# Performance work log

Measured on AMD Instinct MI355X. Metric: run time of the kernel, lower is better.

## Reference

```python
import jax, jax.numpy as jnp
import numpy as np
from jax import lax

G, CPG, KS, N = 8, 8, 3, 9  # groups, channels per group, kernel size, ks*ks


def conv2d(x, w, b=None, pad=1):
    y = lax.conv_general_dilated(x, w, (1, 1), [(pad, pad), (pad, pad)],
                                 dimension_numbers=('NCHW', 'OIHW', 'NCHW'))
    if b is not None:
        y = y + b[None, :, None, None]
    return y


def deform_group(x, f, pw, pb, mw, mb, cw):
    # x: sampled feature (anchor slice), f: offset source (motion slice); both (b,c,h,w)
    b, c, h, w = x.shape
    offset = conv2d(f, pw, pb)                      # (b, 2N, h, w)
    m = jax.nn.sigmoid(conv2d(f, mw, mb))           # (b, N, h, w) modulation
    off = jnp.transpose(offset, (0, 2, 3, 1))       # (b, h, w, 2N): first N rows(x), last N cols(y)
    rng = jnp.arange(-1, 2, dtype=x.dtype)
    pn_x = jnp.repeat(rng, KS)                      # kernel row offset, n = kr*3 + kc
    pn_y = jnp.tile(rng, KS)                        # kernel col offset
    p0_x = jnp.arange(1, h + 1, dtype=x.dtype)[:, None, None]  # base grid starts at 1 (padding=0 here)
    p0_y = jnp.arange(1, w + 1, dtype=x.dtype)[None, :, None]
    px = p0_x + pn_x + off[..., :N]                 # (b, h, w, N)
    py = p0_y + pn_y + off[..., N:]
    fx = jnp.floor(lax.stop_gradient(px))           # p.detach().floor() in the original
    fy = jnp.floor(lax.stop_gradient(py))
    qx_lt = jnp.clip(fx, 0, h - 1)
    qx_rb = jnp.clip(fx + 1, 0, h - 1)
    qy_lt = jnp.clip(fy, 0, w - 1)
    qy_rb = jnp.clip(fy + 1, 0, w - 1)
    px = jnp.clip(px, 0, h - 1)
    py = jnp.clip(py, 0, w - 1)
    g_lt = (1 + (qx_lt - px)) * (1 + (qy_lt - py))
    g_rb = (1 - (qx_rb - px)) * (1 - (qy_rb - py))
    g_lb = (1 + (qx_lt - px)) * (1 - (qy_rb - py))
    g_rt = (1 - (qx_rb - px)) * (1 + (qy_lt - py))
    x_flat = x.reshape(b, c, h * w)

    def gather(ix, iy):
        idx = (ix * w + iy).astype(jnp.int32).reshape(b, 1, -1)  # (b,1,h*w*N)
        return jnp.take_along_axis(x_flat, idx, axis=2).reshape(b, c, h, w, N)

    x_off = (g_lt[:, None] * gather(qx_lt, qy_lt) + g_rb[:, None] * gather(qx_rb, qy_rb)
             + g_lb[:, None] * gather(qx_lt, qy_rb) + g_rt[:, None] * gather(qx_rb, qy_lt))
    x_off = x_off * jnp.transpose(m, (0, 2, 3, 1))[:, None]      # apply modulation mask
    # fused equivalent of reshape to (b,c,h*3,w*3) + conv(k=3, stride=3, no bias)
    return jnp.einsum('bchwn,ocn->bohw', x_off, cw.reshape(cw.shape[0], c, N))


def reference(o, anchor, pw, pb, mw, mb, cw, w1, b1, w2, b2):
    b, C, h, w = anchor.shape
    xg = anchor.reshape(b, G, CPG, h, w).transpose(1, 0, 2, 3, 4)  # (G,b,c,h,w)
    fg = o.reshape(b, G, CPG, h, w).transpose(1, 0, 2, 3, 4)
    tg = jax.vmap(deform_group)(xg, fg, pw, pb, mw, mb, cw)        # (G,b,c,h,w)
    target = tg.transpose(1, 0, 2, 3, 4).reshape(b, C, h, w)
    target_ = jnp.concatenate([target, anchor], axis=1)            # (b,128,h,w)
    return target + conv2d(conv2d(target_, w1, b1), w2, b2)


def setup_inputs() -> dict:
    key = jax.random.key(0)
    ks = jax.random.split(key, 11)
    B, C, H, W = 4, 64, 128, 128
    return {
        'o': jax.random.normal(ks[0], (B, C, H, W), jnp.float32),
        'anchor': jax.random.normal(ks[1], (B, C, H, W), jnp.float32),
        'pw': jax.random.normal(ks[2], (G, 2 * N, CPG, 3, 3), jnp.float32) * 0.05,
        'pb': jax.random.normal(ks[3], (G, 2 * N), jnp.float32) * 0.05,
        'mw': jax.random.normal(ks[4], (G, N, CPG, 3, 3), jnp.float32) * 0.05,
        'mb': jax.random.normal(ks[5], (G, N), jnp.float32) * 0.05,
        'cw': jax.random.normal(ks[6], (G, CPG, CPG, 3, 3), jnp.float32) * 0.05,
        'w1': jax.random.normal(ks[7], (64, 128, 3, 3), jnp.float32) * 0.05,
        'b1': jax.random.normal(ks[8], (64,), jnp.float32) * 0.05,
        'w2': jax.random.normal(ks[9], (64, 64, 3, 3), jnp.float32) * 0.05,
        'b2': jax.random.normal(ks[10], (64,), jnp.float32) * 0.05,
    }
```

## Files before the change

kernel.cpp:

```cpp
#include <hip/hip_runtime.h>


typedef __attribute__((ext_vector_type(8))) short short8;
typedef __attribute__((ext_vector_type(4))) float float4v;
typedef __attribute__((ext_vector_type(2))) float float2v;

#define MFMA_B16(a, b, c) __builtin_amdgcn_mfma_f32_16x16x32_bf16(a, b, c, 0, 0, 0)

__device__ __forceinline__ ushort f2bf(float f) {
    union { float f; unsigned u; } v; v.f = f;
    unsigned r = v.u + 0x7FFFu + ((v.u >> 16) & 1u);
    return (ushort)(r >> 16);
}
__device__ __forceinline__ float bf2f(ushort h) {
    union { unsigned u; float f; } v; v.u = ((unsigned)h) << 16;
    return v.f;
}

__device__ __forceinline__ void tap_wo(int gy, int gx, int n,
                                       float ox, float oy, float mzv,
                                       float* W, int* O)
{
    int ky = n / 3, kx = n - ky * 3;
    float pxf = (float)(gy + ky) + ox;
    float pyf = (float)(gx + kx) + oy;
    float fx = floorf(pxf), fy = floorf(pyf);
    float qxl = fminf(fmaxf(fx, 0.f), 127.f);
    float qxr = fminf(fmaxf(fx + 1.f, 0.f), 127.f);
    float qyl = fminf(fmaxf(fy, 0.f), 127.f);
    float qyr = fminf(fmaxf(fy + 1.f, 0.f), 127.f);
    float pxc = fminf(fmaxf(pxf, 0.f), 127.f);
    float pyc = fminf(fmaxf(pyf, 0.f), 127.f);
    float glx = 1.f + (qxl - pxc), grx = 1.f - (qxr - pxc);
    float gly = 1.f + (qyl - pyc), gry = 1.f - (qyr - pyc);
    float mm = 1.f / (1.f + __expf(-mzv));
    W[0] = glx * gly * mm; W[1] = grx * gry * mm;
    W[2] = glx * gry * mm; W[3] = grx * gly * mm;
    int ixl = (int)qxl, ixr = (int)qxr, iyl = (int)qyl, iyr = (int)qyr;
    O[0] = ixl * 128 + iyl; O[1] = ixr * 128 + iyr;
    O[2] = ixl * 128 + iyr; O[3] = ixr * 128 + iyl;
}

__device__ __forceinline__ short8 interp4(const float* W, const short8* cv)
{
    union U { short8 s; uint4 u; };
    uint4 c[4];
    #pragma unroll
    for (int j = 0; j < 4; ++j) { U t; t.s = cv[j]; c[j] = t.u; }
    U out;
    #pragma unroll
    for (int p = 0; p < 4; ++p) {
        float2v acc = {0.f, 0.f};
        #pragma unroll
        for (int j = 0; j < 4; ++j) {
            unsigned d = (&c[j].x)[p];
            float2v cc = {__uint_as_float(d << 16),
                          __uint_as_float(d & 0xffff0000u)};
            float2v Wv = {W[j], W[j]};
            acc = __builtin_elementwise_fma(cc, Wv, acc);
        }
        unsigned u0 = __float_as_uint(acc.x), u1 = __float_as_uint(acc.y);
        (&out.u.x)[p] = __builtin_amdgcn_perm(u1, u0, 0x07060302u);
    }
    return out.s;
}

__global__ __launch_bounds__(256) void prep(
    const float* __restrict__ anchor,
    const float* __restrict__ w1, const float* __restrict__ w2,
    const float* __restrict__ pw, const float* __restrict__ pb,
    const float* __restrict__ mw, const float* __restrict__ mb,
    const float* __restrict__ cw,
    ushort* __restrict__ anc_g,
    ushort* __restrict__ rw1, ushort* __restrict__ rw2,
    ushort* __restrict__ rpwh, ushort* __restrict__ rpwl,
    ushort* __restrict__ rcw)
{
    const int blk = blockIdx.x;
    if (blk < 256) {
        int pix = (blk & 63) * 256 + threadIdx.x;
        int b = blk >> 6;
        ushort tmp[64];
        #pragma unroll
        for (int ch = 0; ch < 64; ++ch)
            tmp[ch] = f2bf(anchor[(((size_t)(b * 64 + ch)) << 14) + pix]);
        #pragma unroll
        for (int grp = 0; grp < 8; ++grp) {
            short8 v;
            #pragma unroll
            for (int j = 0; j < 8; ++j) v[j] = (short)tmp[grp * 8 + j];
            *(short8*)(anc_g + ((size_t)(b * 8 + grp)) * 131072 + (size_t)pix * 8) = v;
        }
        return;
    }
    int i = (blk - 256) * 256 + threadIdx.x;
    if (i < 73728) {
        int kk = i & 31, r = i >> 5, oc = r & 63, r2 = r >> 6;
        int ks = r2 & 3, s = r2 >> 2, ic = ks * 32 + kk;
        rw1[i] = f2bf(w1[(oc * 128 + ic) * 9 + s]);
    }
    if (i < 36864) {
        int kk = i & 31, r = i >> 5, oc = r & 63, r2 = r >> 6;
        int ks = r2 & 1, s = r2 >> 1, ic = ks * 32 + kk;
        rw2[i] = f2bf(w2[(oc * 64 + ic) * 9 + s]);
    }
    if (i < 24576) {
        int kk = i & 31, r = i >> 5, n = r & 31, r2 = r >> 5;
        int ks = r2 % 3, g = r2 / 3, k = ks * 32 + kk;
        float v = 0.f;
        if (k < 72) {
            int s = k >> 3, ic = k & 7;
            if (n < 18)      v = pw[((g * 18 + n) * 8 + ic) * 9 + s];
            else if (n < 27) v = mw[((g * 9 + (n - 18)) * 8 + ic) * 9 + s];
        } else if (k == 72) {
            if (n < 18)      v = pb[g * 18 + n];
            else if (n < 27) v = mb[g * 9 + (n - 18)];
        }
        ushort h = f2bf(v);
        rpwh[i] = h;
        rpwl[i] = f2bf(v - bf2f(h));
    }
    if (i < 12288) {
        int kk = i & 31, r = i >> 5, oc = r & 15, r2 = r >> 4;
        int ks = r2 % 3, g = r2 / 3, k = ks * 32 + kk;
        float v = 0.f;
        if (k < 72 && oc < 8) {
            int n = k >> 3, ic = k & 7;
            v = cw[((g * 8 + oc) * 8 + ic) * 9 + n];
        }
        rcw[i] = f2bf(v);
    }
}

__global__ __launch_bounds__(256, 4) void deform_mfma(
    const float* __restrict__ o, const ushort* __restrict__ anc_g,
    const ushort* __restrict__ rpwh, const ushort* __restrict__ rpwl,
    const ushort* __restrict__ rcw,
    ushort* __restrict__ xcat_g, float* __restrict__ target)
{
    const int tile = blockIdx.x, g = blockIdx.y, b = blockIdx.z;
    const int ty0 = (tile >> 3) * 16, tx0 = (tile & 7) * 16;
    const int tid = threadIdx.x, lane = tid & 63, wave = tid >> 6;
    const int l15 = lane & 15, quad = lane >> 4;

    __shared__ __align__(16) ushort sU[19008];
    ushort* slabh = sU;
    ushort* slabl = sU + 2592;
    float*  sOff  = (float*)((char*)sU + 10368);
    float*  sEp   = (float*)sU;

    for (int idx = tid; idx < 8 * 324; idx += 256) {
        int ic = idx / 324; int pix = idx - ic * 324;
        int r = pix / 18, c = pix - r * 18;
        int gy = ty0 + r - 1, gx = tx0 + c - 1;
        float v = 0.f;
        if ((unsigned)gy < 128u && (unsigned)gx < 128u)
            v = o[(((size_t)(b * 64 + g * 8 + ic)) << 14) + (gy << 7) + gx];
        ushort h = f2bf(v);
        slabh[pix * 8 + ic] = h;
        slabl[pix * 8 + ic] = f2bf(v - bf2f(h));
    }
    __syncthreads();

    float4v offacc[4][2] = {};
    #pragma unroll
    for (int ks = 0; ks < 3; ++ks) {
        short8 Bh[2], Bl[2];
        #pragma unroll
        for (int nf = 0; nf < 2; ++nf) {
            int off = ((g * 3 + ks) * 32 + nf * 16 + l15) * 32 + quad * 8;
            Bh[nf] = *(const short8*)(rpwh + off);
            Bl[nf] = *(const short8*)(rpwl + off);
        }
        short8 Ah[4], Al[4];
        if (ks < 2) {
            int s = ks * 4 + quad, sy = s / 3, sx = s - sy * 3;
            #pragma unroll
            for (int py = 0; py < 4; ++py) {
                int row = wave * 4 + py;
                int sl = ((row + sy) * 18 + l15 + sx) * 8;
                Ah[py] = *(const short8*)(&slabh[sl]);
                Al[py] = *(const short8*)(&slabl[sl]);
            }
        } else {
            #pragma unroll
            for (int py = 0; py < 4; ++py) {
                short8 zh = {0, 0, 0, 0, 0, 0, 0, 0};
                short8 zl = {0, 0, 0, 0, 0, 0, 0, 0};
                if (quad == 0) {
                    int row = wave * 4 + py;
                    int sl = ((row + 2) * 18 + l15 + 2) * 8;
                    zh = *(const short8*)(&slabh[sl]);
                    zl = *(const short8*)(&slabl[sl]);
                } else if (quad == 1) {
                    zh[0] = (short)0x3F80;
                }
                Ah[py] = zh; Al[py] = zl;
            }
        }
        #pragma unroll
        for (int py = 0; py < 4; ++py)
            #pragma unroll
            for (int nf = 0; nf < 2; ++nf) {
                offacc[py][nf] = MFMA_B16(Ah[py], Bh[nf], offacc[py][nf]);
                offacc[py][nf] = MFMA_B16(Ah[py], Bl[nf], offacc[py][nf]);
                offacc[py][nf] = MFMA_B16(Al[py], Bh[nf], offacc[py][nf]);
            }
    }
    #pragma unroll
    for (int py = 0; py < 4; ++py) {
        int p0 = (wave * 4 + py) * 16 + quad * 4;
        #pragma unroll
        for (int nf = 0; nf < 2; ++nf) {
            int ch = nf * 16 + l15;
            if (ch < 27) {
                #pragma unroll
                for (int reg = 0; reg < 4; ++reg)
                    sOff[(p0 + reg) * 27 + ch] = offacc[py][nf][reg];
            }
        }
    }

    short8 Bw[3];
    #pragma unroll
    for (int ks = 0; ks < 3; ++ks)
        Bw[ks] = *(const short8*)(rcw + (((g * 3 + ks) * 16 + l15) * 32 + quad * 8));

    const ushort* gb = anc_g + ((size_t)(b * 8 + g)) * 131072;
    const int n1 = quad, n2 = quad + 4;
    float4v cacc[4] = {};
    #pragma unroll
    for (int py = 0; py < 4; ++py) {
        int prow = wave * 4 + py;
        int p = prow * 16 + l15;
        int gy = ty0 + prow, gx = tx0 + l15;

        float W[8]; int O[8];
        tap_wo(gy, gx, n1, sOff[p * 27 + n1], sOff[p * 27 + 9 + n1],
               sOff[p * 27 + 18 + n1], &W[0], &O[0]);
        tap_wo(gy, gx, n2, sOff[p * 27 + n2], sOff[p * 27 + 9 + n2],
               sOff[p * 27 + 18 + n2], &W[4], &O[4]);
        short8 cv[8];
        #pragma unroll
        for (int j = 0; j < 8; ++j)
            cv[j] = *(const short8*)(gb + (size_t)O[j] * 8);
        short8 A0 = interp4(&W[0], &cv[0]);
        short8 A1 = interp4(&W[4], &cv[4]);
        short8 A2 = {0, 0, 0, 0, 0, 0, 0, 0};
        if (quad == 0) {
            float W2[4]; int O2[4];
            tap_wo(gy, gx, 8, sOff[p * 27 + 8], sOff[p * 27 + 17],
                   sOff[p * 27 + 26], W2, O2);
            short8 c2[4];
            #pragma unroll
            for (int j = 0; j < 4; ++j)
                c2[j] = *(const short8*)(gb + (size_t)O2[j] * 8);
            A2 = interp4(W2, c2);
        }
        cacc[py] = MFMA_B16(A0, Bw[0], cacc[py]);
        cacc[py] = MFMA_B16(A1, Bw[1], cacc[py]);
        cacc[py] = MFMA_B16(A2, Bw[2], cacc[py]);
    }

    __syncthreads();
    #pragma unroll
    for (int py = 0; py < 4; ++py) {
        if (l15 < 8) {
            #pragma unroll
            for (int reg = 0; reg < 4; ++reg)
                sEp[((wave * 4 + py) * 16 + quad * 4 + reg) * 8 + l15] = cacc[py][reg];
        }
    }
    __syncthreads();
    {
        const int p = tid;
        const int gy = ty0 + (p >> 4), gx = tx0 + (p & 15);
        float res[8];
        #pragma unroll
        for (int oc = 0; oc < 8; ++oc) res[oc] = sEp[p * 8 + oc];
        short8 pk;
        #pragma unroll
        for (int oc = 0; oc < 8; ++oc) pk[oc] = (short)f2bf(res[oc]);
        *(short8*)(xcat_g + ((size_t)(b * 8 + g)) * 131072
                   + (size_t)((gy << 7) + gx) * 8) = pk;
        #pragma unroll
        for (int oc = 0; oc < 8; ++oc)
            target[(((size_t)(b * 64 + g * 8 + oc)) << 14) + (gy << 7) + gx] = res[oc];
    }
}

__global__ __launch_bounds__(256, 4) void conv1_mfma(
    const ushort* __restrict__ xg, const ushort* __restrict__ ag,
    const ushort* __restrict__ rw1, const float* __restrict__ b1,
    ushort* __restrict__ t1)
{
    const int patch = blockIdx.x, b = blockIdx.y;
    const int px0 = (patch & 7) * 16, py0 = (patch >> 3) * 8;
    const int tid = threadIdx.x, lane = tid & 63, wave = tid >> 6;
    const int mhalf = wave & 1, nhalf = wave >> 1;
    const int l15 = lane & 15, quad = lane >> 4;

    __shared__ __align__(16) ushort sA[180 * 72];

    float4v acc[4][2] = {};
    #pragma unroll
    for (int ph = 0; ph < 2; ++ph) {
        if (ph) __syncthreads();
        const ushort* src = (ph == 0) ? xg : ag;
        for (int task = tid; task < 1440; task += 256) {
            int grp = task / 180, pix = task - grp * 180;
            int r = pix / 18, c = pix - r * 18;
            int gy = py0 + r - 1, gx = px0 + c - 1;
            short8 v = {0, 0, 0, 0, 0, 0, 0, 0};
            if ((unsigned)gy < 128u && (unsigned)gx < 128u) {
                const ushort* plane = src + ((size_t)(b * 8 + grp)) * 131072;
                v = *(const short8*)(plane + (size_t)((gy << 7) + gx) * 8);
            }
            *(short8*)(&sA[pix * 72 + grp * 8]) = v;
        }
        __syncthreads();

        #pragma unroll
        for (int ks2 = 0; ks2 < 2; ++ks2) {
            const int ks = ph * 2 + ks2;
            #pragma unroll
            for (int ky = 0; ky < 3; ++ky) {
                short8 Bf[3][2];
                #pragma unroll
                for (int kx = 0; kx < 3; ++kx)
                    #pragma unroll
                    for (int nf = 0; nf < 2; ++nf) {
                        int oc = nhalf * 32 + nf * 16 + l15;
                        Bf[kx][nf] = *(const short8*)(rw1 +
                            ((((ky * 3 + kx) * 4 + ks) * 64 + oc) * 32 + quad * 8));
                    }
                #pragma unroll
                for (int py = 0; py < 4; ++py) {
                    int slabrow = mhalf * 4 + py + ky;
                    #pragma unroll
                    for (int kx = 0; kx < 3; ++kx) {
                        short8 A = *(const short8*)(&sA[(slabrow * 18 + l15 + kx) * 72
                                                        + ks2 * 32 + quad * 8]);
                        #pragma unroll
                        for (int nf = 0; nf < 2; ++nf)
                            acc[py][nf] = MFMA_B16(A, Bf[kx][nf], acc[py][nf]);
                    }
                }
            }
        }
    }
    __syncthreads();
    ushort* sE = sA;
    #pragma unroll
    for (int nf = 0; nf < 2; ++nf) {
        int oc = nhalf * 32 + nf * 16 + l15;
        float bias = b1[oc];
        #pragma unroll
        for (int py = 0; py < 4; ++py) {
            int row = mhalf * 4 + py;
            #pragma unroll
            for (int reg = 0; reg < 4; ++reg)
                sE[(row * 16 + quad * 4 + reg) * 64 + oc] = f2bf(acc[py][nf][reg] + bias);
        }
    }
    __syncthreads();
    {
        const size_t nbase = ((size_t)b) << 20;
        int pix = tid >> 1, half = tid & 1;
        int gy = py0 + (pix >> 4), gx = px0 + (pix & 15);
        ushort* dst = t1 + nbase + (size_t)((gy << 7) + gx) * 64 + half * 32;
        const ushort* sp = sE + pix * 64 + half * 32;
        #pragma unroll
        for (int j = 0; j < 4; ++j)
            *(short8*)(dst + j * 8) = *(const short8*)(sp + j * 8);
    }
}

__global__ __launch_bounds__(256, 4) void conv2_mfma(
    const ushort* __restrict__ t1, const ushort* __restrict__ rw2,
    const float* __restrict__ b2, float* outres)
{
    const int patch = blockIdx.x, b = blockIdx.y;
    const int px0 = (patch & 7) * 16, py0 = (patch >> 3) * 8;
    const int tid = threadIdx.x, lane = tid & 63, wave = tid >> 6;
    const int ohalf = wave & 1, rhalf = wave >> 1;
    const int l15 = lane & 15, quad = lane >> 4;

    __shared__ __align__(16) ushort sX[180 * 72];

    const size_t nbase = ((size_t)b) << 20;
    for (int task = tid; task < 1440; task += 256) {
        int pix = task >> 3, grp = task & 7;
        int r = pix / 18, c = pix - r * 18;
        int gy = py0 + r - 1, gx = px0 + c - 1;
        short8 v = {0, 0, 0, 0, 0, 0, 0, 0};
        if ((unsigned)gy < 128u && (unsigned)gx < 128u)
            v = *(const short8*)(t1 + nbase + (size_t)((gy << 7) + gx) * 64 + grp * 8);
        *(short8*)(&sX[pix * 72 + grp * 8]) = v;
    }
    __syncthreads();

    float4v acc[2][4] = {};
    #pragma unroll
    for (int ks = 0; ks < 2; ++ks) {
        #pragma unroll
        for (int ky = 0; ky < 3; ++ky) {
            short8 Aw[3][2];
            #pragma unroll
            for (int kx = 0; kx < 3; ++kx)
                #pragma unroll
                for (int mf = 0; mf < 2; ++mf) {
                    int oc = ohalf * 32 + mf * 16 + l15;
                    Aw[kx][mf] = *(const short8*)(rw2 +
                        ((((ky * 3 + kx) * 2 + ks) * 64 + oc) * 32 + quad * 8));
                }
            #pragma unroll
            for (int py = 0; py < 4; ++py) {
                int slabrow = rhalf * 4 + py + ky;
                #pragma unroll
                for (int kx = 0; kx < 3; ++kx) {
                    short8 Bx = *(const short8*)(&sX[(slabrow * 18 + l15 + kx) * 72
                                                     + ks * 32 + quad * 8]);
                    #pragma unroll
                    for (int mf = 0; mf < 2; ++mf)
                        acc[mf][py] = MFMA_B16(Aw[kx][mf], Bx, acc[mf][py]);
                }
            }
        }
    }
    #pragma unroll
    for (int mf = 0; mf < 2; ++mf)
        #pragma unroll
        for (int reg = 0; reg < 4; ++reg) {
            int oc = ohalf * 32 + mf * 16 + quad * 4 + reg;
            float bias = b2[oc];
            #pragma unroll
            for (int py = 0; py < 4; ++py) {
                int gy = py0 + rhalf * 4 + py, gx = px0 + l15;
                size_t idx = (((size_t)(b * 64 + oc)) << 14) + (gy << 7) + gx;
                outres[idx] = acc[mf][py][reg] + bias + outres[idx];
            }
        }
}

extern "C" void kernel_launch(void* const* d_in, const int* in_sizes, int n_in,
                              void* d_out, int out_size, void* d_ws, size_t ws_size,
                              hipStream_t stream) {
    const float* o      = (const float*)d_in[0];
    const float* anchor = (const float*)d_in[1];
    const float* pw     = (const float*)d_in[2];
    const float* pb     = (const float*)d_in[3];
    const float* mw     = (const float*)d_in[4];
    const float* mb     = (const float*)d_in[5];
    const float* cw     = (const float*)d_in[6];
    const float* w1     = (const float*)d_in[7];
    const float* b1     = (const float*)d_in[8];
    const float* w2     = (const float*)d_in[9];
    const float* b2     = (const float*)d_in[10];
    float* out = (float*)d_out;

    char* ws = (char*)d_ws;
    ushort* anc_g  = (ushort*)(ws);
    ushort* xcat_g = (ushort*)(ws + 8388608);
    ushort* t1b    = (ushort*)(ws + 16777216);
    char*   wsm    = ws + 25165824;
    ushort* rw1p   = (ushort*)(wsm);
    ushort* rw2p   = (ushort*)(wsm + 147456);
    ushort* rpwh   = (ushort*)(wsm + 147456 + 73728);
    ushort* rpwl   = (ushort*)(wsm + 147456 + 73728 + 49152);
    ushort* rcwp   = (ushort*)(wsm + 147456 + 73728 + 98304);

    prep<<<544, 256, 0, stream>>>(anchor, w1, w2, pw, pb, mw, mb, cw,
                                  anc_g, rw1p, rw2p, rpwh, rpwl, rcwp);
    deform_mfma<<<dim3(64, 8, 4), 256, 0, stream>>>(o, anc_g, rpwh, rpwl, rcwp,
                                                    xcat_g, out );
    conv1_mfma<<<dim3(128, 4), 256, 0, stream>>>(xcat_g, anc_g, rw1p, b1, t1b);
    conv2_mfma<<<dim3(128, 4), 256, 0, stream>>>(t1b, rw2p, b2, out);
}
```

Baseline: 175.1 us.

## Drop fp32 target write; read bf16 residual from xcat in conv2

The deform kernel no longer writes the fp32 target tensor to the output buffer. conv2 instead reads the residual from the bf16 xcat buffer, removing one fp32 write and one fp32 read of the output. The deform slab load now has each thread load all 8 channels of a pixel and store them as packed short8 vectors. The residual added to the output is now bf16-rounded instead of fp32, which reduces accuracy.

```diff
diff --git a/kernel.cpp b/kernel.cpp
--- a/kernel.cpp
+++ b/kernel.cpp
@@ -136,7 +136,7 @@
     const float* __restrict__ o, const ushort* __restrict__ anc_g,
     const ushort* __restrict__ rpwh, const ushort* __restrict__ rpwl,
     const ushort* __restrict__ rcw,
-    ushort* __restrict__ xcat_g, float* __restrict__ target)
+    ushort* __restrict__ xcat_g)
 {
     const int tile = blockIdx.x, g = blockIdx.y, b = blockIdx.z;
     const int ty0 = (tile >> 3) * 16, tx0 = (tile & 7) * 16;
@@ -147,18 +147,30 @@
     ushort* slabh = sU;
     ushort* slabl = sU + 2592;
     float*  sOff  = (float*)((char*)sU + 10368);
-    float*  sEp   = (float*)sU;
-
-    for (int idx = tid; idx < 8 * 324; idx += 256) {
-        int ic = idx / 324; int pix = idx - ic * 324;
-        int r = pix / 18, c = pix - r * 18;
-        int gy = ty0 + r - 1, gx = tx0 + c - 1;
-        float v = 0.f;
-        if ((unsigned)gy < 128u && (unsigned)gx < 128u)
-            v = o[(((size_t)(b * 64 + g * 8 + ic)) << 14) + (gy << 7) + gx];
-        ushort h = f2bf(v);
-        slabh[pix * 8 + ic] = h;
-        slabl[pix * 8 + ic] = f2bf(v - bf2f(h));
+    ushort* sEu   = sU;
+
+    const float* obase = o + (((size_t)(b * 64 + g * 8)) << 14);
+    #pragma unroll
+    for (int pass = 0; pass < 2; ++pass) {
+        int pix = tid + pass * 256;
+        if (pix < 324) {
+            int r = pix / 18, c = pix - r * 18;
+            int gy = ty0 + r - 1, gx = tx0 + c - 1;
+            short8 vh = {0, 0, 0, 0, 0, 0, 0, 0};
+            short8 vl = {0, 0, 0, 0, 0, 0, 0, 0};
+            if ((unsigned)gy < 128u && (unsigned)gx < 128u) {
+                const float* p0 = obase + (gy << 7) + gx;
+                #pragma unroll
+                for (int ic = 0; ic < 8; ++ic) {
+                    float v = p0[(size_t)ic << 14];
+                    ushort h = f2bf(v);
+                    vh[ic] = (short)h;
+                    vl[ic] = (short)f2bf(v - bf2f(h));
+                }
+            }
+            *(short8*)(&slabh[pix * 8]) = vh;
+            *(short8*)(&slabl[pix * 8]) = vl;
+        }
     }
     __syncthreads();
 
@@ -268,24 +280,16 @@
         if (l15 < 8) {
             #pragma unroll
             for (int reg = 0; reg < 4; ++reg)
-                sEp[((wave * 4 + py) * 16 + quad * 4 + reg) * 8 + l15] = cacc[py][reg];
+                sEu[((wave * 4 + py) * 16 + quad * 4 + reg) * 8 + l15] =
+                    f2bf(cacc[py][reg]);
         }
     }
     __syncthreads();
     {
-        const int p = tid;
-        const int gy = ty0 + (p >> 4), gx = tx0 + (p & 15);
-        float res[8];
-        #pragma unroll
-        for (int oc = 0; oc < 8; ++oc) res[oc] = sEp[p * 8 + oc];
-        short8 pk;
-        #pragma unroll
-        for (int oc = 0; oc < 8; ++oc) pk[oc] = (short)f2bf(res[oc]);
+        const int gy = ty0 + (tid >> 4), gx = tx0 + (tid & 15);
+        short8 pk = *(const short8*)(&sEu[tid * 8]);
         *(short8*)(xcat_g + ((size_t)(b * 8 + g)) * 131072
                    + (size_t)((gy << 7) + gx) * 8) = pk;
-        #pragma unroll
-        for (int oc = 0; oc < 8; ++oc)
-            target[(((size_t)(b * 64 + g * 8 + oc)) << 14) + (gy << 7) + gx] = res[oc];
     }
 }
 
@@ -378,7 +382,8 @@
 
 __global__ __launch_bounds__(256, 4) void conv2_mfma(
     const ushort* __restrict__ t1, const ushort* __restrict__ rw2,
-    const float* __restrict__ b2, float* outres)
+    const float* __restrict__ b2, const ushort* __restrict__ xg,
+    float* __restrict__ out)
 {
     const int patch = blockIdx.x, b = blockIdx.y;
     const int px0 = (patch & 7) * 16, py0 = (patch >> 3) * 8;
@@ -434,11 +439,13 @@
         for (int reg = 0; reg < 4; ++reg) {
             int oc = ohalf * 32 + mf * 16 + quad * 4 + reg;
             float bias = b2[oc];
+            const ushort* rplane = xg + ((size_t)(b * 8 + (oc >> 3))) * 131072 + (oc & 7);
             #pragma unroll
             for (int py = 0; py < 4; ++py) {
                 int gy = py0 + rhalf * 4 + py, gx = px0 + l15;
-                size_t idx = (((size_t)(b * 64 + oc)) << 14) + (gy << 7) + gx;
-                outres[idx] = acc[mf][py][reg] + bias + outres[idx];
+                int pix = (gy << 7) + gx;
+                float res = bf2f(rplane[(size_t)pix * 8]);
+                out[(((size_t)(b * 64 + oc)) << 14) + pix] = acc[mf][py][reg] + bias + res;
             }
         }
 }
@@ -473,7 +480,7 @@
     prep<<<544, 256, 0, stream>>>(anchor, w1, w2, pw, pb, mw, mb, cw,
                                   anc_g, rw1p, rw2p, rpwh, rpwl, rcwp);
     deform_mfma<<<dim3(64, 8, 4), 256, 0, stream>>>(o, anc_g, rpwh, rpwl, rcwp,
-                                                    xcat_g, out );
+                                                    xcat_g);
     conv1_mfma<<<dim3(128, 4), 256, 0, stream>>>(xcat_g, anc_g, rw1p, b1, t1b);
-    conv2_mfma<<<dim3(128, 4), 256, 0, stream>>>(t1b, rw2p, b2, out);
-}
+    conv2_mfma<<<dim3(128, 4), 256, 0, stream>>>(t1b, rw2p, b2, xcat_g, out);
+}
```

Result: faster. 164.9 us (-5.8%).
